# Performance work log

Hardware: AMD Instinct MI355X
Metric: run time of the kernel (lower is better)

## Reference

```python
import jax, jax.numpy as jnp
import numpy as np

C = 512
IC = C // 2
BN_EPS = 1e-5

def conv1x1(x, w, b):
    # x: (b,c,h,w), w: (o,c), b: (o,)
    return jnp.einsum('bchw,oc->bohw', x, w) + b[None, :, None, None]

def setup_inputs() -> dict:
    key = jax.random.key(0)
    ks = jax.random.split(key, 9)
    b, h, w = 8, 48, 48
    x = jax.random.normal(ks[0], (b, C, h, w), dtype=jnp.float32)
    s = 1.0 / np.sqrt(C)
    g_w = jax.random.normal(ks[1], (IC, C), dtype=jnp.float32) * s
    g_b = jnp.zeros((IC,), jnp.float32)
    theta_w = jax.random.normal(ks[2], (IC, C), dtype=jnp.float32) * s
    theta_b = jnp.zeros((IC,), jnp.float32)
    phi_w = jax.random.normal(ks[3], (IC, C), dtype=jnp.float32) * s
    phi_b = jnp.zeros((IC,), jnp.float32)
    w_w = jax.random.normal(ks[4], (C, IC), dtype=jnp.float32) * (1.0 / np.sqrt(IC))
    w_b = jnp.zeros((C,), jnp.float32)
    # BatchNorm affine params: initialized to 0 per nn.init.constant_ in source
    bn_gamma = jnp.zeros((C,), jnp.float32)
    bn_beta = jnp.zeros((C,), jnp.float32)
    return {"x": x, "g_w": g_w, "g_b": g_b, "theta_w": theta_w, "theta_b": theta_b,
            "phi_w": phi_w, "phi_b": phi_b, "w_w": w_w, "w_b": w_b,
            "bn_gamma": bn_gamma, "bn_beta": bn_beta}

def reference(x, g_w, g_b, theta_w, theta_b, phi_w, phi_b, w_w, w_b, bn_gamma, bn_beta):
    b, c, h, w = x.shape
    hw = h * w
    g_x = conv1x1(x, g_w, g_b).reshape(b, IC, hw).transpose(0, 2, 1)      # (b,hw,ic)
    theta_x = conv1x1(x, theta_w, theta_b).reshape(b, IC, hw).transpose(0, 2, 1)  # (b,hw,ic)
    phi_x = conv1x1(x, phi_w, phi_b).reshape(b, IC, hw)                    # (b,ic,hw)
    f = jnp.einsum('bqc,bck->bqk', theta_x, phi_x)                         # (b,hw,hw), unscaled
    f_div_C = jax.nn.softmax(f, axis=-1)
    y = jnp.einsum('bqk,bkc->bqc', f_div_C, g_x)                           # (b,hw,ic)
    y = y.transpose(0, 2, 1).reshape(b, IC, h, w)
    wy = conv1x1(y, w_w, w_b)                                              # (b,c,h,w)
    # BatchNorm2d in training mode: batch statistics over (b,h,w)
    mean = jnp.mean(wy, axis=(0, 2, 3), keepdims=True)
    var = jnp.var(wy, axis=(0, 2, 3), keepdims=True)
    wy_bn = (wy - mean) / jnp.sqrt(var + BN_EPS)
    wy_bn = wy_bn * bn_gamma[None, :, None, None] + bn_beta[None, :, None, None]
    return wy_bn + x
```

## Files before the change

kernel.cpp:

```cpp
#include <hip/hip_runtime.h>
#include <hip/hip_bf16.h>
#include <stdint.h>

constexpr int Bn  = 8;
constexpr int Cc  = 512;
constexpr int ICc = 256;
constexpr int HWc = 48 * 48;
constexpr float BN_EPS = 1e-5f;

typedef unsigned short u16;
typedef __attribute__((ext_vector_type(8))) short short8;
typedef __attribute__((ext_vector_type(4))) float f32x4;

__device__ __forceinline__ u16 f2bf(float f) {
    uint32_t u = __builtin_bit_cast(uint32_t, f);
    u += 0x7fffu + ((u >> 16) & 1u);
    return (u16)(u >> 16);
}
__device__ __forceinline__ float bf2f(u16 h) {
    uint32_t u = ((uint32_t)h) << 16;
    return __builtin_bit_cast(float, u);
}
__device__ __forceinline__ void load_lds16(const void* g, void* l) {
    __builtin_amdgcn_global_load_lds(
        (const __attribute__((address_space(1))) void*)(uintptr_t)g,
        (__attribute__((address_space(3))) void*)(uintptr_t)l, 16, 0, 0);
}

__global__ __launch_bounds__(256)
void cast3_weights(const float* __restrict__ a, const float* __restrict__ b,
                   const float* __restrict__ c, u16* __restrict__ out) {
    int idx = blockIdx.x * 256 + threadIdx.x;
    int which = idx >> 15, off = idx & 32767;
    const float4* src = (which == 0 ? (const float4*)a
                        : which == 1 ? (const float4*)b : (const float4*)c) + off;
    float4 v = *src;
    ushort4 o;
    o.x = f2bf(v.x); o.y = f2bf(v.y); o.z = f2bf(v.z); o.w = f2bf(v.w);
    ((ushort4*)out)[idx] = o;
}

__global__ __launch_bounds__(256)
void cast1_weight(const float* __restrict__ a, u16* __restrict__ out) {
    int idx = blockIdx.x * 256 + threadIdx.x;
    float4 v = ((const float4*)a)[idx];
    ushort4 o;
    o.x = f2bf(v.x); o.y = f2bf(v.y); o.z = f2bf(v.z); o.w = f2bf(v.w);
    ((ushort4*)out)[idx] = o;
}

__global__ __launch_bounds__(256)
void transpose_cast_x(const float* __restrict__ x, u16* __restrict__ xt) {
    __shared__ float t[32][33];
    const int b = blockIdx.z;
    const int p0 = blockIdx.x * 32;
    const int c0 = blockIdx.y * 32;
    const int tx = threadIdx.x & 31, ty = threadIdx.x >> 5;
    const float* xb = x + (size_t)b * Cc * HWc;
#pragma unroll
    for (int r = 0; r < 32; r += 8)
        t[ty + r][tx] = xb[(size_t)(c0 + ty + r) * HWc + p0 + tx];
    __syncthreads();
    u16* xtb = xt + (size_t)b * HWc * Cc;
#pragma unroll
    for (int r = 0; r < 32; r += 8)
        xtb[(size_t)(p0 + ty + r) * Cc + c0 + tx] = f2bf(t[tx][ty + r]);
}

template <int STORE>
__global__ __launch_bounds__(256, 2)
void mfma_gemm(const u16* __restrict__ A, const u16* __restrict__ B,
               void* __restrict__ Cout, const float* __restrict__ bias,
               int bias_mode, int K, int ldA, int ldB, int ldC,
               size_t sA, size_t sB, size_t sC) {
    __shared__ __align__(16) u16 As[128 * 32];
    __shared__ __align__(16) u16 Bs[128 * 32];
    const int bz = blockIdx.z;
    const int m0 = blockIdx.y * 128, n0 = blockIdx.x * 128;
    const u16* Ab = A + (size_t)bz * sA + (size_t)m0 * ldA;
    const u16* Bb = B + (size_t)bz * sB + (size_t)n0 * ldB;
    const int tid = threadIdx.x, lane = tid & 63, w = tid >> 6;
    const int wm = (w & 1) * 64, wn = (w >> 1) * 64;
    const int quad = lane >> 4, m16 = lane & 15;

    f32x4 acc[4][4];
#pragma unroll
    for (int i = 0; i < 4; ++i)
#pragma unroll
        for (int j = 0; j < 4; ++j) acc[i][j] = (f32x4){0.f, 0.f, 0.f, 0.f};

    const int L0 = 2 * w * 64 + lane;
    const int L1 = L0 + 64;
    const int r0 = L0 >> 2, c0 = (L0 & 3) * 8;
    const int r1 = L1 >> 2, c1 = (L1 & 3) * 8;

    for (int k0 = 0; k0 < K; k0 += 32) {
        load_lds16(Ab + (size_t)r0 * ldA + k0 + c0, &As[2 * w * 512]);
        load_lds16(Ab + (size_t)r1 * ldA + k0 + c1, &As[(2 * w + 1) * 512]);
        load_lds16(Bb + (size_t)r0 * ldB + k0 + c0, &Bs[2 * w * 512]);
        load_lds16(Bb + (size_t)r1 * ldB + k0 + c1, &Bs[(2 * w + 1) * 512]);
        __syncthreads();

        short8 af[4], bfv[4];
#pragma unroll
        for (int i = 0; i < 4; ++i)
            af[i] = *(const short8*)&As[(wm + i * 16 + m16) * 32 + quad * 8];
#pragma unroll
        for (int j = 0; j < 4; ++j)
            bfv[j] = *(const short8*)&Bs[(wn + j * 16 + m16) * 32 + quad * 8];
#pragma unroll
        for (int i = 0; i < 4; ++i)
#pragma unroll
            for (int j = 0; j < 4; ++j)
                acc[i][j] = __builtin_amdgcn_mfma_f32_16x16x32_bf16(
                    af[i], bfv[j], acc[i][j], 0, 0, 0);
        __syncthreads();
    }

    if (STORE == 0) {
        u16* C = (u16*)Cout + (size_t)bz * sC;
#pragma unroll
        for (int i = 0; i < 4; ++i) {
            int m = m0 + wm + i * 16 + quad * 4;
#pragma unroll
            for (int j = 0; j < 4; ++j) {
                int n = n0 + wn + j * 16 + m16;
                float bn_ = (bias_mode == 1) ? bias[n] : 0.f;
#pragma unroll
                for (int r = 0; r < 4; ++r) {
                    float v = acc[i][j][r] +
                              ((bias_mode == 2) ? bias[m + r] : bn_);
                    C[(size_t)(m + r) * ldC + n] = f2bf(v);
                }
            }
        }
    } else {
        float* C = (float*)Cout + (size_t)bz * sC;
#pragma unroll
        for (int i = 0; i < 4; ++i) {
            int m = m0 + wm + i * 16 + quad * 4;
#pragma unroll
            for (int j = 0; j < 4; ++j) {
                int n = n0 + wn + j * 16 + m16;
                float bn_ = (bias_mode == 1) ? bias[n] : 0.f;
#pragma unroll
                for (int r = 0; r < 4; ++r) {
                    float v = acc[i][j][r] +
                              ((bias_mode == 2) ? bias[m + r] : bn_);
                    C[(size_t)(m + r) * ldC + n] = v;
                }
            }
        }
    }
}

__global__ __launch_bounds__(192)
void softmax_rows(u16* __restrict__ S) {
    const int b = blockIdx.x & 7;
    const int q = blockIdx.x >> 3;
    u16* row = S + ((size_t)b * HWc + q) * (size_t)HWc;
    const int tid = threadIdx.x;

    float v[12];
#pragma unroll
    for (int c = 0; c < 3; ++c) {
        uint2 raw = *(const uint2*)&row[(c * 192 + tid) * 4];
        v[c * 4 + 0] = bf2f((u16)(raw.x & 0xffff));
        v[c * 4 + 1] = bf2f((u16)(raw.x >> 16));
        v[c * 4 + 2] = bf2f((u16)(raw.y & 0xffff));
        v[c * 4 + 3] = bf2f((u16)(raw.y >> 16));
    }
    float m = v[0];
#pragma unroll
    for (int i = 1; i < 12; ++i) m = fmaxf(m, v[i]);
#pragma unroll
    for (int off = 32; off; off >>= 1) m = fmaxf(m, __shfl_down(m, off, 64));
    __shared__ float redm[3], reds[3];
    if ((tid & 63) == 0) redm[tid >> 6] = m;
    __syncthreads();
    m = fmaxf(fmaxf(redm[0], redm[1]), redm[2]);

    float s = 0.f;
#pragma unroll
    for (int i = 0; i < 12; ++i) { v[i] = __expf(v[i] - m); s += v[i]; }
#pragma unroll
    for (int off = 32; off; off >>= 1) s += __shfl_down(s, off, 64);
    if ((tid & 63) == 0) reds[tid >> 6] = s;
    __syncthreads();
    const float rinv = 1.0f / (reds[0] + reds[1] + reds[2]);

#pragma unroll
    for (int c = 0; c < 3; ++c) {
        uint2 o;
        o.x = (uint32_t)f2bf(v[c * 4 + 0] * rinv) |
              ((uint32_t)f2bf(v[c * 4 + 1] * rinv) << 16);
        o.y = (uint32_t)f2bf(v[c * 4 + 2] * rinv) |
              ((uint32_t)f2bf(v[c * 4 + 3] * rinv) << 16);
        *(uint2*)&row[(c * 192 + tid) * 4] = o;
    }
}

__global__ __launch_bounds__(256)
void bn_stats(const float* __restrict__ wy, float* __restrict__ stats) {
    const int o = blockIdx.x;
    const int tid = threadIdx.x;
    float s0 = 0.f, s1 = 0.f;
    for (int b = 0; b < Bn; ++b) {
        const float* r = wy + (size_t)b * Cc * HWc + (size_t)o * HWc;
        for (int p = tid; p < HWc; p += 256) {
            float v = r[p];
            s0 += v;
            s1 = fmaf(v, v, s1);
        }
    }
#pragma unroll
    for (int off = 32; off; off >>= 1) {
        s0 += __shfl_down(s0, off, 64);
        s1 += __shfl_down(s1, off, 64);
    }
    __shared__ float r0[4], r1[4];
    if ((tid & 63) == 0) { r0[tid >> 6] = s0; r1[tid >> 6] = s1; }
    __syncthreads();
    if (tid == 0) {
        float sum = r0[0] + r0[1] + r0[2] + r0[3];
        float sq  = r1[0] + r1[1] + r1[2] + r1[3];
        const float N = (float)(Bn * HWc);
        float mean = sum / N;
        float var  = sq / N - mean * mean;
        stats[o]      = mean;
        stats[Cc + o] = rsqrtf(var + BN_EPS);
    }
}

__global__ __launch_bounds__(256)
void bn_apply(const float* __restrict__ wy, const float* __restrict__ x,
              const float* __restrict__ stats, const float* __restrict__ gamma,
              const float* __restrict__ beta, float* __restrict__ out) {
    const size_t i4 = (size_t)blockIdx.x * 256 + threadIdx.x;
    const size_t base = i4 * 4;
    const int o = (int)((base / HWc) % Cc);
    const float mean = stats[o];
    const float rstd = stats[Cc + o];
    const float ga = gamma[o];
    const float be = beta[o];
    const float4 w4 = ((const float4*)wy)[i4];
    const float4 x4 = ((const float4*)x)[i4];
    float4 r;
    r.x = (w4.x - mean) * rstd * ga + be + x4.x;
    r.y = (w4.y - mean) * rstd * ga + be + x4.y;
    r.z = (w4.z - mean) * rstd * ga + be + x4.z;
    r.w = (w4.w - mean) * rstd * ga + be + x4.w;
    ((float4*)out)[i4] = r;
}

extern "C" void kernel_launch(void* const* d_in, const int* in_sizes, int n_in,
                              void* d_out, int out_size, void* d_ws, size_t ws_size,
                              hipStream_t stream) {
    const float* x     = (const float*)d_in[0];
    const float* g_w   = (const float*)d_in[1];
    const float* g_b   = (const float*)d_in[2];
    const float* th_w  = (const float*)d_in[3];
    const float* th_b  = (const float*)d_in[4];
    const float* ph_w  = (const float*)d_in[5];
    const float* ph_b  = (const float*)d_in[6];
    const float* w_w   = (const float*)d_in[7];
    const float* w_b   = (const float*)d_in[8];
    const float* gamma = (const float*)d_in[9];
    const float* beta  = (const float*)d_in[10];

    char* base = (char*)d_ws;
    const size_t SZT = (size_t)Bn * HWc * ICc * 2;
    u16* tht = (u16*)base;
    u16* pht = (u16*)(base + SZT);
    u16* g   = (u16*)(base + 2 * SZT);
    char* Sreg = base + 3 * SZT;
    u16* S    = (u16*)Sreg;
    u16* xt   = (u16*)Sreg;
    u16* wbf1 = (u16*)(Sreg + (size_t)Bn * HWc * Cc * 2);
    u16* y    = (u16*)base;
    float* wy = (float*)Sreg;
    u16* wbf2 = (u16*)(Sreg + (size_t)Bn * Cc * HWc * 4);
    float* stats = (float*)(Sreg + (size_t)Bn * Cc * HWc * 4 + 262144);

    dim3 blk(256);

    cast3_weights<<<dim3(384), blk, 0, stream>>>(th_w, ph_w, g_w, wbf1);
    transpose_cast_x<<<dim3(HWc / 32, Cc / 32, Bn), blk, 0, stream>>>(x, xt);

    const u16* thwb = wbf1;
    const u16* phwb = wbf1 + 131072;
    const u16* gwb  = wbf1 + 262144;

    mfma_gemm<0><<<dim3(2, 18, Bn), blk, 0, stream>>>(
        xt, thwb, tht, th_b, 1, Cc, Cc, Cc, ICc,
        (size_t)HWc * Cc, 0, (size_t)HWc * ICc);
    mfma_gemm<0><<<dim3(2, 18, Bn), blk, 0, stream>>>(
        xt, phwb, pht, ph_b, 1, Cc, Cc, Cc, ICc,
        (size_t)HWc * Cc, 0, (size_t)HWc * ICc);
    mfma_gemm<0><<<dim3(18, 2, Bn), blk, 0, stream>>>(
        gwb, xt, g, g_b, 2, Cc, Cc, Cc, HWc,
        0, (size_t)HWc * Cc, (size_t)ICc * HWc);

    mfma_gemm<0><<<dim3(18, 18, Bn), blk, 0, stream>>>(
        tht, pht, S, nullptr, 0, ICc, ICc, ICc, HWc,
        (size_t)HWc * ICc, (size_t)HWc * ICc, (size_t)HWc * HWc);

    softmax_rows<<<dim3(Bn * HWc), dim3(192), 0, stream>>>(S);

    mfma_gemm<0><<<dim3(2, 18, Bn), blk, 0, stream>>>(
        S, g, y, nullptr, 0, HWc, HWc, HWc, ICc,
        (size_t)HWc * HWc, (size_t)ICc * HWc, (size_t)HWc * ICc);

    cast1_weight<<<dim3(128), blk, 0, stream>>>(w_w, wbf2);

    mfma_gemm<1><<<dim3(18, 4, Bn), blk, 0, stream>>>(
        wbf2, y, wy, w_b, 2, ICc, ICc, ICc, HWc,
        0, (size_t)HWc * ICc, (size_t)Cc * HWc);

    bn_stats<<<dim3(Cc), blk, 0, stream>>>(wy, stats);
    bn_apply<<<dim3((Bn * Cc * HWc) / 4 / 256), blk, 0, stream>>>(
        wy, x, stats, gamma, beta, (float*)d_out);
}
```

Baseline: 376.6 us.

## Merge theta/phi projections, fuse BN stats into GEMM epilogue, add 64-row tiles

```diff
diff --git a/kernel.cpp b/kernel.cpp
--- a/kernel.cpp
+++ b/kernel.cpp
@@ -28,20 +28,28 @@
 }
 
 __global__ __launch_bounds__(256)
-void cast3_weights(const float* __restrict__ a, const float* __restrict__ b,
-                   const float* __restrict__ c, u16* __restrict__ out) {
+void cast_front(const float* __restrict__ th_w, const float* __restrict__ ph_w,
+                const float* __restrict__ g_w, const float* __restrict__ th_b,
+                const float* __restrict__ ph_b, u16* __restrict__ wcat,
+                float* __restrict__ bias_thph) {
     int idx = blockIdx.x * 256 + threadIdx.x;
-    int which = idx >> 15, off = idx & 32767;
-    const float4* src = (which == 0 ? (const float4*)a
-                        : which == 1 ? (const float4*)b : (const float4*)c) + off;
-    float4 v = *src;
-    ushort4 o;
-    o.x = f2bf(v.x); o.y = f2bf(v.y); o.z = f2bf(v.z); o.w = f2bf(v.w);
-    ((ushort4*)out)[idx] = o;
+    if (idx < 98304) {
+        const float4* src;
+        if (idx < 32768)       src = (const float4*)th_w + idx;
+        else if (idx < 65536)  src = (const float4*)ph_w + (idx - 32768);
+        else                   src = (const float4*)g_w  + (idx - 65536);
+        float4 v = *src;
+        ushort4 o;
+        o.x = f2bf(v.x); o.y = f2bf(v.y); o.z = f2bf(v.z); o.w = f2bf(v.w);
+        ((ushort4*)wcat)[idx] = o;
+    } else if (idx < 98816) {
+        int i = idx - 98304;
+        bias_thph[i] = (i < 256) ? th_b[i] : ph_b[i - 256];
+    }
 }
 
 __global__ __launch_bounds__(256)
-void cast1_weight(const float* __restrict__ a, u16* __restrict__ out) {
+void cast_w(const float* __restrict__ a, u16* __restrict__ out) {
     int idx = blockIdx.x * 256 + threadIdx.x;
     float4 v = ((const float4*)a)[idx];
     ushort4 o;
@@ -51,65 +59,79 @@
 
 __global__ __launch_bounds__(256)
 void transpose_cast_x(const float* __restrict__ x, u16* __restrict__ xt) {
-    __shared__ float t[32][33];
+    __shared__ float t[64][33];
     const int b = blockIdx.z;
     const int p0 = blockIdx.x * 32;
-    const int c0 = blockIdx.y * 32;
+    const int c0 = blockIdx.y * 64;
     const int tx = threadIdx.x & 31, ty = threadIdx.x >> 5;
     const float* xb = x + (size_t)b * Cc * HWc;
 #pragma unroll
-    for (int r = 0; r < 32; r += 8)
-        t[ty + r][tx] = xb[(size_t)(c0 + ty + r) * HWc + p0 + tx];
+    for (int r = 0; r < 8; ++r)
+        t[r * 8 + ty][tx] = xb[(size_t)(c0 + r * 8 + ty) * HWc + p0 + tx];
     __syncthreads();
     u16* xtb = xt + (size_t)b * HWc * Cc;
-#pragma unroll
-    for (int r = 0; r < 32; r += 8)
-        xtb[(size_t)(p0 + ty + r) * Cc + c0 + tx] = f2bf(t[tx][ty + r]);
-}
-
-template <int STORE>
+    const int cc = (threadIdx.x & 31) * 2, pp = threadIdx.x >> 5;
+#pragma unroll
+    for (int r = 0; r < 4; ++r) {
+        int p = r * 8 + pp;
+        ushort2 v;
+        v.x = f2bf(t[cc][p]);
+        v.y = f2bf(t[cc + 1][p]);
+        *(ushort2*)&xtb[(size_t)(p0 + p) * Cc + c0 + cc] = v;
+    }
+}
+
+template <int TM, int STORE, bool STATS>
 __global__ __launch_bounds__(256, 2)
 void mfma_gemm(const u16* __restrict__ A, const u16* __restrict__ B,
                void* __restrict__ Cout, const float* __restrict__ bias,
                int bias_mode, int K, int ldA, int ldB, int ldC,
-               size_t sA, size_t sB, size_t sC) {
-    __shared__ __align__(16) u16 As[128 * 32];
+               size_t sA, size_t sB, size_t sC,
+               float* __restrict__ s0g, float* __restrict__ s1g) {
+    constexpr int MI = TM / 32;
+    __shared__ __align__(16) u16 As[TM * 32];
     __shared__ __align__(16) u16 Bs[128 * 32];
     const int bz = blockIdx.z;
-    const int m0 = blockIdx.y * 128, n0 = blockIdx.x * 128;
+    const int m0 = blockIdx.y * TM, n0 = blockIdx.x * 128;
     const u16* Ab = A + (size_t)bz * sA + (size_t)m0 * ldA;
     const u16* Bb = B + (size_t)bz * sB + (size_t)n0 * ldB;
     const int tid = threadIdx.x, lane = tid & 63, w = tid >> 6;
-    const int wm = (w & 1) * 64, wn = (w >> 1) * 64;
+    const int wm = (w & 1) * (TM / 2);
+    const int wn = (w >> 1) * 64;
     const int quad = lane >> 4, m16 = lane & 15;
 
-    f32x4 acc[4][4];
-#pragma unroll
-    for (int i = 0; i < 4; ++i)
+    f32x4 acc[MI][4];
+#pragma unroll
+    for (int i = 0; i < MI; ++i)
 #pragma unroll
         for (int j = 0; j < 4; ++j) acc[i][j] = (f32x4){0.f, 0.f, 0.f, 0.f};
 
-    const int L0 = 2 * w * 64 + lane;
-    const int L1 = L0 + 64;
-    const int r0 = L0 >> 2, c0 = (L0 & 3) * 8;
-    const int r1 = L1 >> 2, c1 = (L1 & 3) * 8;
+    const int L0 = 2 * w * 64 + lane, L1 = L0 + 64;
+    const int br0 = L0 >> 2, bc0 = (L0 & 3) * 8;
+    const int br1 = L1 >> 2, bc1 = (L1 & 3) * 8;
+    const int ar0 = (TM == 128) ? br0 : (tid >> 2);
+    const int ac0 = (TM == 128) ? bc0 : (tid & 3) * 8;
 
     for (int k0 = 0; k0 < K; k0 += 32) {
-        load_lds16(Ab + (size_t)r0 * ldA + k0 + c0, &As[2 * w * 512]);
-        load_lds16(Ab + (size_t)r1 * ldA + k0 + c1, &As[(2 * w + 1) * 512]);
-        load_lds16(Bb + (size_t)r0 * ldB + k0 + c0, &Bs[2 * w * 512]);
-        load_lds16(Bb + (size_t)r1 * ldB + k0 + c1, &Bs[(2 * w + 1) * 512]);
+        if (TM == 128) {
+            load_lds16(Ab + (size_t)ar0 * ldA + k0 + ac0, &As[2 * w * 512]);
+            load_lds16(Ab + (size_t)br1 * ldA + k0 + bc1, &As[(2 * w + 1) * 512]);
+        } else {
+            load_lds16(Ab + (size_t)ar0 * ldA + k0 + ac0, &As[w * 512]);
+        }
+        load_lds16(Bb + (size_t)br0 * ldB + k0 + bc0, &Bs[2 * w * 512]);
+        load_lds16(Bb + (size_t)br1 * ldB + k0 + bc1, &Bs[(2 * w + 1) * 512]);
         __syncthreads();
 
-        short8 af[4], bfv[4];
-#pragma unroll
-        for (int i = 0; i < 4; ++i)
+        short8 af[MI], bfv[4];
+#pragma unroll
+        for (int i = 0; i < MI; ++i)
             af[i] = *(const short8*)&As[(wm + i * 16 + m16) * 32 + quad * 8];
 #pragma unroll
         for (int j = 0; j < 4; ++j)
             bfv[j] = *(const short8*)&Bs[(wn + j * 16 + m16) * 32 + quad * 8];
 #pragma unroll
-        for (int i = 0; i < 4; ++i)
+        for (int i = 0; i < MI; ++i)
 #pragma unroll
             for (int j = 0; j < 4; ++j)
                 acc[i][j] = __builtin_amdgcn_mfma_f32_16x16x32_bf16(
@@ -117,37 +139,67 @@
         __syncthreads();
     }
 
+    if (bias_mode) {
+#pragma unroll
+        for (int i = 0; i < MI; ++i)
+#pragma unroll
+            for (int j = 0; j < 4; ++j)
+#pragma unroll
+                for (int r = 0; r < 4; ++r)
+                    acc[i][j][r] += (bias_mode == 2)
+                        ? bias[m0 + wm + i * 16 + quad * 4 + r]
+                        : bias[n0 + wn + j * 16 + m16];
+    }
+
     if (STORE == 0) {
         u16* C = (u16*)Cout + (size_t)bz * sC;
 #pragma unroll
-        for (int i = 0; i < 4; ++i) {
+        for (int i = 0; i < MI; ++i) {
             int m = m0 + wm + i * 16 + quad * 4;
 #pragma unroll
             for (int j = 0; j < 4; ++j) {
                 int n = n0 + wn + j * 16 + m16;
-                float bn_ = (bias_mode == 1) ? bias[n] : 0.f;
-#pragma unroll
-                for (int r = 0; r < 4; ++r) {
-                    float v = acc[i][j][r] +
-                              ((bias_mode == 2) ? bias[m + r] : bn_);
-                    C[(size_t)(m + r) * ldC + n] = f2bf(v);
-                }
+#pragma unroll
+                for (int r = 0; r < 4; ++r)
+                    C[(size_t)(m + r) * ldC + n] = f2bf(acc[i][j][r]);
             }
         }
     } else {
         float* C = (float*)Cout + (size_t)bz * sC;
 #pragma unroll
-        for (int i = 0; i < 4; ++i) {
+        for (int i = 0; i < MI; ++i) {
             int m = m0 + wm + i * 16 + quad * 4;
 #pragma unroll
             for (int j = 0; j < 4; ++j) {
                 int n = n0 + wn + j * 16 + m16;
-                float bn_ = (bias_mode == 1) ? bias[n] : 0.f;
-#pragma unroll
-                for (int r = 0; r < 4; ++r) {
-                    float v = acc[i][j][r] +
-                              ((bias_mode == 2) ? bias[m + r] : bn_);
-                    C[(size_t)(m + r) * ldC + n] = v;
+#pragma unroll
+                for (int r = 0; r < 4; ++r)
+                    C[(size_t)(m + r) * ldC + n] = acc[i][j][r];
+            }
+        }
+    }
+
+    if (STATS) {
+#pragma unroll
+        for (int i = 0; i < MI; ++i) {
+#pragma unroll
+            for (int r = 0; r < 4; ++r) {
+                float v0 = 0.f, v1 = 0.f;
+#pragma unroll
+                for (int j = 0; j < 4; ++j) {
+                    float v = acc[i][j][r];
+                    v0 += v;
+                    v1 = fmaf(v, v, v1);
+                }
+#pragma unroll
+                for (int off = 8; off; off >>= 1) {
+                    v0 += __shfl_down(v0, off, 16);
+                    v1 += __shfl_down(v1, off, 16);
+                }
+                if (m16 == 0) {
+                    int m = m0 + wm + i * 16 + quad * 4 + r;
+                    atomicAdd(&s0g[m], v0);
+                    atomicAdd(&s1g[m], v1);
                 }
             }
         }
@@ -201,46 +253,17 @@
 }
 
 __global__ __launch_bounds__(256)
-void bn_stats(const float* __restrict__ wy, float* __restrict__ stats) {
-    const int o = blockIdx.x;
-    const int tid = threadIdx.x;
-    float s0 = 0.f, s1 = 0.f;
-    for (int b = 0; b < Bn; ++b) {
-        const float* r = wy + (size_t)b * Cc * HWc + (size_t)o * HWc;
-        for (int p = tid; p < HWc; p += 256) {
-            float v = r[p];
-            s0 += v;
-            s1 = fmaf(v, v, s1);
-        }
-    }
-#pragma unroll
-    for (int off = 32; off; off >>= 1) {
-        s0 += __shfl_down(s0, off, 64);
-        s1 += __shfl_down(s1, off, 64);
-    }
-    __shared__ float r0[4], r1[4];
-    if ((tid & 63) == 0) { r0[tid >> 6] = s0; r1[tid >> 6] = s1; }
-    __syncthreads();
-    if (tid == 0) {
-        float sum = r0[0] + r0[1] + r0[2] + r0[3];
-        float sq  = r1[0] + r1[1] + r1[2] + r1[3];
-        const float N = (float)(Bn * HWc);
-        float mean = sum / N;
-        float var  = sq / N - mean * mean;
-        stats[o]      = mean;
-        stats[Cc + o] = rsqrtf(var + BN_EPS);
-    }
-}
-
-__global__ __launch_bounds__(256)
 void bn_apply(const float* __restrict__ wy, const float* __restrict__ x,
-              const float* __restrict__ stats, const float* __restrict__ gamma,
-              const float* __restrict__ beta, float* __restrict__ out) {
+              const float* __restrict__ s0, const float* __restrict__ s1,
+              const float* __restrict__ gamma, const float* __restrict__ beta,
+              float* __restrict__ out) {
     const size_t i4 = (size_t)blockIdx.x * 256 + threadIdx.x;
     const size_t base = i4 * 4;
     const int o = (int)((base / HWc) % Cc);
-    const float mean = stats[o];
-    const float rstd = stats[Cc + o];
+    const float N = (float)(Bn * HWc);
+    const float mean = s0[o] / N;
+    const float var  = s1[o] / N - mean * mean;
+    const float rstd = rsqrtf(var + BN_EPS);
     const float ga = gamma[o];
     const float be = beta[o];
     const float4 w4 = ((const float4*)wy)[i4];
@@ -270,54 +293,53 @@
 
     char* base = (char*)d_ws;
     const size_t SZT = (size_t)Bn * HWc * ICc * 2;
-    u16* tht = (u16*)base;
-    u16* pht = (u16*)(base + SZT);
-    u16* g   = (u16*)(base + 2 * SZT);
+    u16* thph = (u16*)base;
+    u16* g    = (u16*)(base + 2 * SZT);
     char* Sreg = base + 3 * SZT;
     u16* S    = (u16*)Sreg;
     u16* xt   = (u16*)Sreg;
-    u16* wbf1 = (u16*)(Sreg + (size_t)Bn * HWc * Cc * 2);
+    u16* wcat = (u16*)(Sreg + (size_t)Bn * HWc * Cc * 2);
+    float* bias_thph = (float*)(Sreg + (size_t)Bn * HWc * Cc * 2 + 786432);
     u16* y    = (u16*)base;
+    u16* wbf2 = (u16*)(base + SZT);
+    float* stats = (float*)(base + SZT + 262144);
     float* wy = (float*)Sreg;
-    u16* wbf2 = (u16*)(Sreg + (size_t)Bn * Cc * HWc * 4);
-    float* stats = (float*)(Sreg + (size_t)Bn * Cc * HWc * 4 + 262144);
 
     dim3 blk(256);
-
-    cast3_weights<<<dim3(384), blk, 0, stream>>>(th_w, ph_w, g_w, wbf1);
-    transpose_cast_x<<<dim3(HWc / 32, Cc / 32, Bn), blk, 0, stream>>>(x, xt);
-
-    const u16* thwb = wbf1;
-    const u16* phwb = wbf1 + 131072;
-    const u16* gwb  = wbf1 + 262144;
-
-    mfma_gemm<0><<<dim3(2, 18, Bn), blk, 0, stream>>>(
-        xt, thwb, tht, th_b, 1, Cc, Cc, Cc, ICc,
-        (size_t)HWc * Cc, 0, (size_t)HWc * ICc);
-    mfma_gemm<0><<<dim3(2, 18, Bn), blk, 0, stream>>>(
-        xt, phwb, pht, ph_b, 1, Cc, Cc, Cc, ICc,
-        (size_t)HWc * Cc, 0, (size_t)HWc * ICc);
-    mfma_gemm<0><<<dim3(18, 2, Bn), blk, 0, stream>>>(
+    const u16* thphw = wcat;
+    const u16* gwb   = wcat + 262144;
+
+    cast_front<<<dim3(386), blk, 0, stream>>>(th_w, ph_w, g_w, th_b, ph_b,
+                                              wcat, bias_thph);
+    transpose_cast_x<<<dim3(HWc / 32, Cc / 64, Bn), blk, 0, stream>>>(x, xt);
+
+    mfma_gemm<128, 0, false><<<dim3(4, 18, Bn), blk, 0, stream>>>(
+        xt, thphw, thph, bias_thph, 1, Cc, Cc, Cc, 512,
+        (size_t)HWc * Cc, 0, (size_t)HWc * 512, nullptr, nullptr);
+
+    mfma_gemm<64, 0, false><<<dim3(18, 4, Bn), blk, 0, stream>>>(
         gwb, xt, g, g_b, 2, Cc, Cc, Cc, HWc,
-        0, (size_t)HWc * Cc, (size_t)ICc * HWc);
-
-    mfma_gemm<0><<<dim3(18, 18, Bn), blk, 0, stream>>>(
-        tht, pht, S, nullptr, 0, ICc, ICc, ICc, HWc,
-        (size_t)HWc * ICc, (size_t)HWc * ICc, (size_t)HWc * HWc);
+        0, (size_t)HWc * Cc, (size_t)ICc * HWc, nullptr, nullptr);
+
+    mfma_gemm<128, 0, false><<<dim3(18, 18, Bn), blk, 0, stream>>>(
+        thph, thph + 256, S, nullptr, 0, ICc, 512, 512, HWc,
+        (size_t)HWc * 512, (size_t)HWc * 512, (size_t)HWc * HWc,
+        nullptr, nullptr);
+
+    cast_w<<<dim3(128), blk, 0, stream>>>(w_w, wbf2);
+    hipMemsetAsync(stats, 0, 2 * Cc * sizeof(float), stream);
 
     softmax_rows<<<dim3(Bn * HWc), dim3(192), 0, stream>>>(S);
 
-    mfma_gemm<0><<<dim3(2, 18, Bn), blk, 0, stream>>>(
+    mfma_gemm<64, 0, false><<<dim3(2, 36, Bn), blk, 0, stream>>>(
         S, g, y, nullptr, 0, HWc, HWc, HWc, ICc,
-        (size_t)HWc * HWc, (size_t)ICc * HWc, (size_t)HWc * ICc);
-
-    cast1_weight<<<dim3(128), blk, 0, stream>>>(w_w, wbf2);
-
-    mfma_gemm<1><<<dim3(18, 4, Bn), blk, 0, stream>>>(
+        (size_t)HWc * HWc, (size_t)ICc * HWc, (size_t)HWc * ICc,
+        nullptr, nullptr);
+
+    mfma_gemm<128, 1, true><<<dim3(18, 4, Bn), blk, 0, stream>>>(
         wbf2, y, wy, w_b, 2, ICc, ICc, ICc, HWc,
-        0, (size_t)HWc * ICc, (size_t)Cc * HWc);
-
-    bn_stats<<<dim3(Cc), blk, 0, stream>>>(wy, stats);
+        0, (size_t)HWc * ICc, (size_t)Cc * HWc, stats, stats + Cc);
+
     bn_apply<<<dim3((Bn * Cc * HWc) / 4 / 256), blk, 0, stream>>>(
-        wy, x, stats, gamma, beta, (float*)d_out);
-}
+        wy, x, stats, stats + Cc, gamma, beta, (float*)d_out);
+}
```

New measurement: 341.1 us. 1.1x faster.
